# Kernel tuning notes

Hardware: AMD Instinct MI355X
Metric: run time of the kernel (lower is better)

Reference implementation:

```python
import jax, jax.numpy as jnp
import numpy as np

N = 100000       # nodes
E = 3200000      # edges
F_IN = 128       # num_node_features
DIM = 32         # hidden dim (fixed in Net1)
L = 3            # num_layers
C = 10           # num_classes


def setup_inputs() -> dict:
    key = jax.random.key(0)
    ks = jax.random.split(key, 16)
    x = jax.random.normal(ks[0], (N, F_IN), dtype=jnp.float32)
    src = jax.random.randint(ks[1], (E,), 0, N, dtype=jnp.int32)
    dst = jax.random.randint(ks[2], (E,), 0, N, dtype=jnp.int32)
    def glorot(k, shape):
        lim = np.sqrt(6.0 / (shape[0] + shape[1])).astype(np.float32)
        return jax.random.uniform(k, shape, jnp.float32, -lim, lim)
    dims = [F_IN, DIM, DIM]
    inp = {"x": x, "src": src, "dst": dst}
    for i in range(L):
        din = dims[i]
        inp[f"Wn{i}"] = glorot(ks[3 + 3 * i], (din, DIM))      # neighbor weight
        inp[f"bn{i}"] = jnp.zeros((DIM,), jnp.float32)          # neighbor bias
        inp[f"Ws{i}"] = glorot(ks[4 + 3 * i], (din, DIM))      # self weight (no bias)
    inp["fc_w"] = glorot(ks[13], (DIM * L + F_IN, C))
    inp["fc_b"] = jnp.zeros((C,), jnp.float32)
    return inp


def _graph_conv_wl(x, src, dst, Wn, bn, Ws):
    # GraphConv(norm='none'): transform then aggregate (sum over in-neighbors)
    h = x @ Wn                                   # [N, DIM]
    msg = h[src]                                 # [E, DIM] gather
    agg = jax.ops.segment_sum(msg, dst, num_segments=N)  # [N, DIM] scatter-add
    return agg + bn + x @ Ws


def reference(x, src, dst, Wn0, bn0, Ws0, Wn1, bn1, Ws1, Wn2, bn2, Ws2, fc_w, fc_b):
    params = [(Wn0, bn0, Ws0), (Wn1, bn1, Ws1), (Wn2, bn2, Ws2)]
    xs = [x]
    h = x
    for Wn, bn, Ws in params:
        h = jax.nn.relu(_graph_conv_wl(h, src, dst, Wn, bn, Ws))
        xs.append(h)
    h = jnp.concatenate(xs, axis=1)              # [N, 128 + 3*32]
    logits = h @ fc_w + fc_b                     # [N, C]
    return jax.nn.log_softmax(logits, axis=1)
```

## Files before the change

kernel.cpp:

```cpp
#include <hip/hip_runtime.h>
#include <cstdint>

#define NN 100000
#define EE 3200000
#define SB_BITS 8
#define SB_NODES (1 << SB_BITS)
#define NSB ((NN + SB_NODES - 1) / SB_NODES)
#define CAP 9216
#define CH 4096
#define EPT (CH / 256)

__device__ inline float4 add4(float4 a, float4 b) {
    return make_float4(a.x + b.x, a.y + b.y, a.z + b.z, a.w + b.w);
}


__global__ void k_hist_sb(const int* __restrict__ dst, int* __restrict__ scnt) {
    __shared__ int h[NSB];
    for (int i = threadIdx.x; i < NSB; i += 256) h[i] = 0;
    __syncthreads();
    for (int e = blockIdx.x * 256 + threadIdx.x; e < EE; e += gridDim.x * 256)
        atomicAdd(&h[dst[e] >> SB_BITS], 1);
    __syncthreads();
    for (int i = threadIdx.x; i < NSB; i += 256) {
        int v = h[i];
        if (v) atomicAdd(&scnt[i], v);
    }
}

__global__ void k_scan_sb(const int* __restrict__ scnt,
                          int* __restrict__ sbptr, int* __restrict__ cursor) {
    __shared__ int sm[512];
    int i = threadIdx.x;
    int v0 = (i < NSB) ? scnt[i] : 0;
    int v1 = (i + 256 < NSB) ? scnt[i + 256] : 0;
    sm[i] = v0;
    sm[i + 256] = v1;
    __syncthreads();
    for (int o = 1; o < 512; o <<= 1) {
        int a0 = (i >= o) ? sm[i - o] : 0;
        int a1 = (i + 256 >= o) ? sm[i + 256 - o] : 0;
        __syncthreads();
        sm[i] += a0;
        sm[i + 256] += a1;
        __syncthreads();
    }
    if (i < NSB)       { sbptr[i]       = sm[i] - v0;       cursor[i]       = sm[i] - v0; }
    if (i + 256 < NSB) { sbptr[i + 256] = sm[i + 256] - v1; cursor[i + 256] = sm[i + 256] - v1; }
    if (i == 0) sbptr[NSB] = sm[511];
}

__global__ void k_split(const int* __restrict__ src, const int* __restrict__ dst,
                        int* __restrict__ cursor, int* __restrict__ out) {
    __shared__ int hist[512];
    __shared__ int lbase[NSB];
    __shared__ int gbase[NSB];
    __shared__ int buf[CH];
    __shared__ unsigned short keyb[CH];
    const int nchunks = (EE + CH - 1) / CH;
    for (int c = blockIdx.x; c < nchunks; c += gridDim.x) {
        int base = c * CH;
        int cnt = min(CH, EE - base);
        hist[threadIdx.x] = 0;
        hist[threadIdx.x + 256] = 0;
        __syncthreads();
        int words[EPT], ranks[EPT], keys[EPT];
        #pragma unroll
        for (int k = 0; k < EPT; ++k) {
            int idx = threadIdx.x + k * 256;
            if (idx < cnt) {
                int d = dst[base + idx];
                int s = src[base + idx];
                int key = d >> SB_BITS;
                words[k] = s | ((d & (SB_NODES - 1)) << 17);
                keys[k] = key;
                ranks[k] = atomicAdd(&hist[key], 1);
            } else keys[k] = -1;
        }
        __syncthreads();
        int i = threadIdx.x;
        int v0 = hist[i], v1 = hist[i + 256];
        for (int o = 1; o < 512; o <<= 1) {
            int a0 = (i >= o) ? hist[i - o] : 0;
            int a1 = (i + 256 >= o) ? hist[i + 256 - o] : 0;
            __syncthreads();
            hist[i] += a0;
            hist[i + 256] += a1;
            __syncthreads();
        }
        if (i < NSB) {
            lbase[i] = hist[i] - v0;
            gbase[i] = (v0 > 0) ? atomicAdd(&cursor[i], v0) : 0;
        }
        if (i + 256 < NSB) {
            lbase[i + 256] = hist[i + 256] - v1;
            gbase[i + 256] = (v1 > 0) ? atomicAdd(&cursor[i + 256], v1) : 0;
        }
        __syncthreads();
        #pragma unroll
        for (int k = 0; k < EPT; ++k) {
            if (keys[k] >= 0) {
                int p = lbase[keys[k]] + ranks[k];
                buf[p] = words[k];
                keyb[p] = (unsigned short)keys[k];
            }
        }
        __syncthreads();
        for (int j = threadIdx.x; j < cnt; j += 256) {
            int kk = keyb[j];
            out[gbase[kk] + (j - lbase[kk])] = buf[j];
        }
        __syncthreads();
    }
}

__global__ void k_sb_sort(const int* __restrict__ sbptr, const int* __restrict__ packed,
                          int* __restrict__ csr_src, int* __restrict__ rowptr) {
    __shared__ int hist[SB_NODES];
    __shared__ int lbuf[CAP];
    int b = blockIdx.x;
    int e0 = sbptr[b], e1 = sbptr[b + 1];
    int cnt = e1 - e0;
    hist[threadIdx.x] = 0;
    __syncthreads();
    for (int j = e0 + threadIdx.x; j < e1; j += 256)
        atomicAdd(&hist[(packed[j] >> 17) & (SB_NODES - 1)], 1);
    __syncthreads();
    int i = threadIdx.x;
    int v = hist[i];
    for (int o = 1; o < 256; o <<= 1) {
        int a = (i >= o) ? hist[i - o] : 0;
        __syncthreads();
        hist[i] += a;
        __syncthreads();
    }
    int excl = hist[i] - v;
    int node = (b << SB_BITS) + i;
    if (node < NN) rowptr[node] = e0 + excl;
    hist[i] = excl;
    if (b == 0 && i == 0) rowptr[NN] = EE;
    __syncthreads();
    if (cnt <= CAP) {
        for (int j = e0 + threadIdx.x; j < e1; j += 256) {
            int w = packed[j];
            int n = (w >> 17) & (SB_NODES - 1);
            int pos = atomicAdd(&hist[n], 1);
            lbuf[pos] = w & 0x1FFFF;
        }
        __syncthreads();
        for (int j = threadIdx.x; j < cnt; j += 256)
            csr_src[e0 + j] = lbuf[j];
    } else {
        for (int j = e0 + threadIdx.x; j < e1; j += 256) {
            int w = packed[j];
            int n = (w >> 17) & (SB_NODES - 1);
            int pos = atomicAdd(&hist[n], 1);
            csr_src[e0 + pos] = w & 0x1FFFF;
        }
    }
}


__global__ void k_transform(const float* __restrict__ h,
                            const float* __restrict__ Wn,
                            const float* __restrict__ Ws,
                            const float* __restrict__ bn,
                            float* __restrict__ t,
                            float* __restrict__ hout,
                            int din) {
    __shared__ float WnL[128 * 32];
    __shared__ float WsL[128 * 32];
    for (int i = threadIdx.x; i < din * 32; i += 256) {
        WnL[i] = Wn[i];
        WsL[i] = Ws[i];
    }
    __syncthreads();
    int node = blockIdx.x * 8 + (threadIdx.x >> 5);
    int d = threadIdx.x & 31;
    if (node >= NN) return;
    const float* hr = h + (size_t)node * din;
    float accn = 0.f;
    float accs = bn[d];
    for (int k = 0; k < din; ++k) {
        float f = hr[k];
        accn += f * WnL[k * 32 + d];
        accs += f * WsL[k * 32 + d];
    }
    t[node * 32 + d] = accn;
    hout[node * 32 + d] = accs;
}

__global__ void k_aggregate(const int* __restrict__ rowptr,
                            const int* __restrict__ csr_src,
                            const float4* __restrict__ t4,
                            float4* __restrict__ hout4) {
    int node = blockIdx.x * 32 + (threadIdx.x >> 3);
    int q = threadIdx.x & 7;
    if (node >= NN) return;
    int j = rowptr[node];
    int end = rowptr[node + 1];
    float4 a0 = make_float4(0.f, 0.f, 0.f, 0.f);
    float4 a1 = a0, a2 = a0, a3 = a0;
    for (; j + 4 <= end; j += 4) {
        int s0 = csr_src[j];
        int s1 = csr_src[j + 1];
        int s2 = csr_src[j + 2];
        int s3 = csr_src[j + 3];
        a0 = add4(a0, t4[s0 * 8 + q]);
        a1 = add4(a1, t4[s1 * 8 + q]);
        a2 = add4(a2, t4[s2 * 8 + q]);
        a3 = add4(a3, t4[s3 * 8 + q]);
    }
    for (; j < end; ++j) a0 = add4(a0, t4[csr_src[j] * 8 + q]);
    float4 s = add4(add4(a0, a1), add4(a2, a3));
    int idx = node * 8 + q;
    float4 h = hout4[idx];
    h.x = fmaxf(h.x + s.x, 0.f);
    h.y = fmaxf(h.y + s.y, 0.f);
    h.z = fmaxf(h.z + s.z, 0.f);
    h.w = fmaxf(h.w + s.w, 0.f);
    hout4[idx] = h;
}

__global__ void k_final(const float* __restrict__ x,
                        const float* __restrict__ h1,
                        const float* __restrict__ h2,
                        const float* __restrict__ h3,
                        const float* __restrict__ fc_w,
                        const float* __restrict__ fc_b,
                        float* __restrict__ out) {
    __shared__ float Wl[224 * 10];
    __shared__ float bl[10];
    for (int i = threadIdx.x; i < 224 * 10; i += blockDim.x) Wl[i] = fc_w[i];
    if (threadIdx.x < 10) bl[threadIdx.x] = fc_b[threadIdx.x];
    __syncthreads();
    int n = blockIdx.x * blockDim.x + threadIdx.x;
    if (n >= NN) return;
    float acc[10];
    #pragma unroll
    for (int c = 0; c < 10; ++c) acc[c] = bl[c];
    const float* xr = x + (size_t)n * 128;
    for (int j = 0; j < 128; ++j) {
        float f = xr[j];
        #pragma unroll
        for (int c = 0; c < 10; ++c) acc[c] += f * Wl[j * 10 + c];
    }
    const float* hs[3] = {h1, h2, h3};
    for (int l = 0; l < 3; ++l) {
        const float* hr = hs[l] + (size_t)n * 32;
        for (int j = 0; j < 32; ++j) {
            float f = hr[j];
            #pragma unroll
            for (int c = 0; c < 10; ++c) acc[c] += f * Wl[(128 + l * 32 + j) * 10 + c];
        }
    }
    float m = acc[0];
    #pragma unroll
    for (int c = 1; c < 10; ++c) m = fmaxf(m, acc[c]);
    float s = 0.f;
    #pragma unroll
    for (int c = 0; c < 10; ++c) s += __expf(acc[c] - m);
    float ls = __logf(s);
    #pragma unroll
    for (int c = 0; c < 10; ++c) out[n * 10 + c] = acc[c] - m - ls;
}

extern "C" void kernel_launch(void* const* d_in, const int* in_sizes, int n_in,
                              void* d_out, int out_size, void* d_ws, size_t ws_size,
                              hipStream_t stream) {
    const float* x   = (const float*)d_in[0];
    const int*   src = (const int*)d_in[1];
    const int*   dst = (const int*)d_in[2];
    const float* Wn[3] = {(const float*)d_in[3], (const float*)d_in[6], (const float*)d_in[9]};
    const float* bn[3] = {(const float*)d_in[4], (const float*)d_in[7], (const float*)d_in[10]};
    const float* Ws[3] = {(const float*)d_in[5], (const float*)d_in[8], (const float*)d_in[11]};
    const float* fc_w = (const float*)d_in[12];
    const float* fc_b = (const float*)d_in[13];
    float* out = (float*)d_out;

    char* w = (char*)d_ws;
    const size_t NF = (size_t)NN * 32;
    float* t   = (float*)w;                     w += NF * 4;
    float* h1  = (float*)w;                     w += NF * 4;
    float* h2  = (float*)w;                     w += NF * 4;
    float* h3  = (float*)w;                     w += NF * 4;
    int* csr_src = (int*)w;                     w += (size_t)EE * 4;
    int* scnt   = (int*)w;                      w += (size_t)NSB * 4;
    int* sbptr  = (int*)w;                      w += (size_t)(NSB + 1) * 4;
    int* cursor = (int*)w;                      w += (size_t)NSB * 4;
    int* rowptr = (int*)w;                      w += (size_t)(NN + 1) * 4;
    int* packed = (int*)h3;
    float* hbuf[3] = {h1, h2, h3};

    hipMemsetAsync(scnt, 0, (size_t)NSB * 4, stream);
    k_hist_sb<<<512, 256, 0, stream>>>(dst, scnt);
    k_scan_sb<<<1, 256, 0, stream>>>(scnt, sbptr, cursor);
    k_split<<<512, 256, 0, stream>>>(src, dst, cursor, packed);
    k_sb_sort<<<NSB, 256, 0, stream>>>(sbptr, packed, csr_src, rowptr);

    const int mm_blocks = (NN + 7) / 8;
    const int ag_blocks = (NN + 31) / 32;
    const float* hin = x;
    int din = 128;
    for (int l = 0; l < 3; ++l) {
        k_transform<<<mm_blocks, 256, 0, stream>>>(hin, Wn[l], Ws[l], bn[l], t, hbuf[l], din);
        k_aggregate<<<ag_blocks, 256, 0, stream>>>(rowptr, csr_src, (const float4*)t, (float4*)hbuf[l]);
        hin = hbuf[l];
        din = 32;
    }
    k_final<<<(NN + 255) / 256, 256, 0, stream>>>(x, h1, h2, h3, fc_w, fc_b, out);
}
```

Before: 527.7 us.

## Restructure node transform to one thread per node with register accumulators

Rewrites the dense transform kernel so that each thread computes all 32 outputs of one node. Each wavefront handles 64 nodes for either the neighbor weight or the self weight. Weight rows are read with wave-uniform loads, no longer staged in shared memory, and input rows are read as float4. Outputs are written as float4 vectors. The goal is to drop the shared-memory weight staging and the per-FMA LDS reads, at the cost of reading each input row twice (once per weight) and strided, uncoalesced row loads across lanes.

```diff
diff --git a/kernel.cpp b/kernel.cpp
--- a/kernel.cpp
+++ b/kernel.cpp
@@ -161,33 +161,47 @@
 }
 
 
-__global__ void k_transform(const float* __restrict__ h,
-                            const float* __restrict__ Wn,
-                            const float* __restrict__ Ws,
-                            const float* __restrict__ bn,
-                            float* __restrict__ t,
-                            float* __restrict__ hout,
-                            int din) {
-    __shared__ float WnL[128 * 32];
-    __shared__ float WsL[128 * 32];
-    for (int i = threadIdx.x; i < din * 32; i += 256) {
-        WnL[i] = Wn[i];
-        WsL[i] = Ws[i];
-    }
-    __syncthreads();
-    int node = blockIdx.x * 8 + (threadIdx.x >> 5);
-    int d = threadIdx.x & 31;
-    if (node >= NN) return;
-    const float* hr = h + (size_t)node * din;
-    float accn = 0.f;
-    float accs = bn[d];
-    for (int k = 0; k < din; ++k) {
-        float f = hr[k];
-        accn += f * WnL[k * 32 + d];
-        accs += f * WsL[k * 32 + d];
-    }
-    t[node * 32 + d] = accn;
-    hout[node * 32 + d] = accs;
+__global__ __launch_bounds__(256) void k_transform(
+        const float* __restrict__ h,
+        const float* __restrict__ Wn,
+        const float* __restrict__ Ws,
+        const float* __restrict__ bn,
+        float* __restrict__ t,
+        float* __restrict__ hout,
+        int din) {
+    int wid = (blockIdx.x * 256 + threadIdx.x) >> 6;
+    int lane = threadIdx.x & 63;
+    int which = wid & 1;
+    int node = (wid >> 1) * 64 + lane;
+    bool valid = node < NN;
+    int nclamp = valid ? node : NN - 1;
+    const float* __restrict__ W = which ? Ws : Wn;
+    const float* __restrict__ hr = h + (size_t)nclamp * din;
+    float acc[32];
+    #pragma unroll
+    for (int d = 0; d < 32; ++d) acc[d] = 0.f;
+    for (int k = 0; k < din; k += 4) {
+        float4 f = *(const float4*)(hr + k);
+        const float* __restrict__ w0 = W + k * 32;
+        #pragma unroll
+        for (int d = 0; d < 32; ++d) acc[d] = fmaf(f.x, w0[d], acc[d]);
+        #pragma unroll
+        for (int d = 0; d < 32; ++d) acc[d] = fmaf(f.y, w0[32 + d], acc[d]);
+        #pragma unroll
+        for (int d = 0; d < 32; ++d) acc[d] = fmaf(f.z, w0[64 + d], acc[d]);
+        #pragma unroll
+        for (int d = 0; d < 32; ++d) acc[d] = fmaf(f.w, w0[96 + d], acc[d]);
+    }
+    if (valid) {
+        if (which) {
+            #pragma unroll
+            for (int d = 0; d < 32; ++d) acc[d] += bn[d];
+        }
+        float* __restrict__ dstp = (which ? hout : t) + (size_t)node * 32;
+        #pragma unroll
+        for (int d = 0; d < 32; d += 4)
+            *(float4*)(dstp + d) = make_float4(acc[d], acc[d + 1], acc[d + 2], acc[d + 3]);
+    }
 }
 
 __global__ void k_aggregate(const int* __restrict__ rowptr,
@@ -298,12 +312,13 @@
     k_split<<<512, 256, 0, stream>>>(src, dst, cursor, packed);
     k_sb_sort<<<NSB, 256, 0, stream>>>(sbptr, packed, csr_src, rowptr);
 
-    const int mm_blocks = (NN + 7) / 8;
+    const int tr_waves = 2 * ((NN + 63) / 64);
+    const int tr_blocks = (tr_waves * 64 + 255) / 256;
     const int ag_blocks = (NN + 31) / 32;
     const float* hin = x;
     int din = 128;
     for (int l = 0; l < 3; ++l) {
-        k_transform<<<mm_blocks, 256, 0, stream>>>(hin, Wn[l], Ws[l], bn[l], t, hbuf[l], din);
+        k_transform<<<tr_blocks, 256, 0, stream>>>(hin, Wn[l], Ws[l], bn[l], t, hbuf[l], din);
         k_aggregate<<<ag_blocks, 256, 0, stream>>>(rowptr, csr_src, (const float4*)t, (float4*)hbuf[l]);
         hin = hbuf[l];
         din = 32;
```

After: 593.3 us. 12.4% more time.
